# Performance work log

Measured on AMD Instinct MI355X. Metric: run time of the kernel, lower is better.

The kernel has to match this reference:

```python
import jax, jax.numpy as jnp
import numpy as np

D = 512; H = 8; DH = D // H; DFF = 4 * D; INNER = 2 * D; K = 31
B = 8; S = 1024
EPS = 1e-5


def layer_norm(x, g, b):
    m = jnp.mean(x, axis=-1, keepdims=True)
    v = jnp.mean(jnp.square(x - m), axis=-1, keepdims=True)
    return (x - m) * jax.lax.rsqrt(v + EPS) * g + b


def setup_inputs() -> dict:
    key = jax.random.key(0)
    ks = iter(jax.random.split(key, 32))
    w = lambda *s: jax.random.normal(next(ks), s, dtype=jnp.float32) * 0.02
    d = {
        "x": jax.random.normal(next(ks), (B, S, D), dtype=jnp.float32),
        # FF module 1
        "ln1_g": jnp.ones((D,)), "ln1_b": jnp.zeros((D,)),
        "ff1_w1": w(DFF, D), "ff1_b1": jnp.zeros((DFF,)),
        "ff1_w2": w(D, DFF), "ff1_b2": jnp.zeros((D,)),
        # attention
        "lna_g": jnp.ones((D,)), "lna_b": jnp.zeros((D,)),
        "qkv_w": w(3 * D, D), "qkv_b": jnp.zeros((3 * D,)),
        "out_w": w(D, D), "out_b": jnp.zeros((D,)),
        # conv module
        "lnc_g": jnp.ones((D,)), "lnc_b": jnp.zeros((D,)),
        "pw1_w": w(INNER, D), "pw1_b": jnp.zeros((INNER,)),
        "dw_w": w(D, 1, K), "dw_b": jnp.zeros((D,)),
        "bn_g": jnp.ones((D,)), "bn_b": jnp.zeros((D,)),
        "bn_mean": jnp.zeros((D,)), "bn_var": jnp.ones((D,)),
        "pw2_w": w(D, D), "pw2_b": jnp.zeros((D,)),
        # FF module 2
        "ln2_g": jnp.ones((D,)), "ln2_b": jnp.zeros((D,)),
        "ff2_w1": w(DFF, D), "ff2_b1": jnp.zeros((DFF,)),
        "ff2_w2": w(D, DFF), "ff2_b2": jnp.zeros((D,)),
        # final layer norm
        "lnf_g": jnp.ones((D,)), "lnf_b": jnp.zeros((D,)),
    }
    return d


def _ff(x, g, b, w1, b1, w2, b2):
    h = layer_norm(x, g, b)
    h = jax.nn.silu(h @ w1.T + b1)
    h = h @ w2.T + b2
    return h + x  # FeedForwardModule adds its own residual


def _attn(x, g, b, qkv_w, qkv_b, out_w, out_b):
    h = layer_norm(x, g, b)
    qkv = (h @ qkv_w.T + qkv_b).reshape(B, S, 3, H, DH)
    q, k, v = qkv[:, :, 0], qkv[:, :, 1], qkv[:, :, 2]  # [B,S,H,DH]
    scores = jnp.einsum('bqhd,bkhd->bhqk', q, k) / np.sqrt(DH).astype(np.float32)
    probs = jax.nn.softmax(scores, axis=-1)
    ctx = jnp.einsum('bhqk,bkhd->bqhd', probs, v).reshape(B, S, D)
    return ctx @ out_w.T + out_b


def _conv(x, g, b, pw1_w, pw1_b, dw_w, dw_b, bn_g, bn_b, bn_mean, bn_var, pw2_w, pw2_b):
    h = layer_norm(x, g, b)
    y = h @ pw1_w.T + pw1_b                      # [B,S,2D] pointwise conv1
    a, gate = jnp.split(y, 2, axis=-1)           # GLU along channel dim
    y = a * jax.nn.sigmoid(gate)                 # [B,S,D]
    y = y.transpose(0, 2, 1)                     # [B,D,S]
    y = jax.lax.conv_general_dilated(
        y, dw_w, window_strides=(1,), padding=((K // 2, K // 2),),
        dimension_numbers=('NCH', 'OIH', 'NCH'), feature_group_count=D)
    y = y + dw_b[None, :, None]
    y = (y - bn_mean[None, :, None]) * jax.lax.rsqrt(bn_var + EPS)[None, :, None]
    y = y * bn_g[None, :, None] + bn_b[None, :, None]
    y = jax.nn.silu(y)
    y = y.transpose(0, 2, 1)                     # [B,S,D]
    y = y @ pw2_w.T + pw2_b
    return y + x  # ConvModule adds its own residual


def reference(x, ln1_g, ln1_b, ff1_w1, ff1_b1, ff1_w2, ff1_b2,
              lna_g, lna_b, qkv_w, qkv_b, out_w, out_b,
              lnc_g, lnc_b, pw1_w, pw1_b, dw_w, dw_b,
              bn_g, bn_b, bn_mean, bn_var, pw2_w, pw2_b,
              ln2_g, ln2_b, ff2_w1, ff2_b1, ff2_w2, ff2_b2,
              lnf_g, lnf_b):
    x = x + 0.5 * _ff(x, ln1_g, ln1_b, ff1_w1, ff1_b1, ff1_w2, ff1_b2)
    x = x + _attn(x, lna_g, lna_b, qkv_w, qkv_b, out_w, out_b)
    x = x + _conv(x, lnc_g, lnc_b, pw1_w, pw1_b, dw_w, dw_b,
                  bn_g, bn_b, bn_mean, bn_var, pw2_w, pw2_b)
    x = x + 0.5 * _ff(x, ln2_g, ln2_b, ff2_w1, ff2_b1, ff2_w2, ff2_b2)
    return layer_norm(x, lnf_g, lnf_b)
```

## Files before the change

### kernel.cpp

```cpp
#include <hip/hip_runtime.h>
#include <hip/hip_bf16.h>

typedef __attribute__((ext_vector_type(8))) short bf16x8;
typedef __attribute__((ext_vector_type(4))) float f32x4;

#define NTOK 8192
#define SEQ  1024
#define NH   8

__device__ __forceinline__ float bfs2f(short s) {
  union { unsigned u; float f; } x; x.u = ((unsigned)(unsigned short)s) << 16; return x.f;
}
__device__ __forceinline__ short f2bfs(float f) {
  __hip_bfloat16 h = __float2bfloat16(f);
  return *reinterpret_cast<short*>(&h);
}
__device__ __forceinline__ float bfp2f(const __hip_bfloat16* p) {
  return bfs2f(*reinterpret_cast<const short*>(p));
}

__device__ __forceinline__ void gld16(const void* g, void* l) {
  __builtin_amdgcn_global_load_lds(
      (__attribute__((address_space(1))) void*)const_cast<void*>(g),
      (__attribute__((address_space(3))) void*)l, 16, 0, 0);
}

struct WSeg { const float* src; unsigned dst_off; unsigned nvec; };
struct WPack { WSeg s[8]; };

__global__ __launch_bounds__(256) void cast_wall_kernel(WPack p,
                                                        __hip_bfloat16* __restrict__ dst) {
  unsigned v = blockIdx.x * 256 + threadIdx.x;
#pragma unroll
  for (int t = 0; t < 8; ++t) {
    if (v < p.s[t].nvec) {
      const float* s = p.s[t].src + (size_t)v * 8;
      f32x4 a = *reinterpret_cast<const f32x4*>(s);
      f32x4 b = *reinterpret_cast<const f32x4*>(s + 4);
      bf16x8 o;
#pragma unroll
      for (int j = 0; j < 4; ++j) { o[j] = f2bfs(a[j]); o[4 + j] = f2bfs(b[j]); }
      *reinterpret_cast<bf16x8*>(reinterpret_cast<short*>(dst) +
                                 (size_t)(p.s[t].dst_off + v) * 8) = o;
      return;
    }
    v -= p.s[t].nvec;
  }
}

__global__ __launch_bounds__(256) void cast_dww_kernel(const float* __restrict__ src,
                                                       __hip_bfloat16* __restrict__ dst) {
  for (int k = 0; k < 31; ++k)
    for (int c = threadIdx.x; c < 512; c += 256)
      dst[k * 512 + c] = __float2bfloat16(src[c * 31 + k]);
}

struct PtrPack { const void* p[23]; };

__global__ __launch_bounds__(256) void cast_small_kernel(PtrPack pk,
                                                         __hip_bfloat16* __restrict__ dst) {
  constexpr int sizes[23] = {512, 512, 2048, 512, 512, 512, 1536, 512, 512, 512, 1024, 512,
                             512, 512, 512, 512, 512, 512, 512, 2048, 512, 512, 512};
  int off = 0;
  for (int t = 0; t < 23; ++t) {
    const int n = sizes[t];
    for (int i = threadIdx.x; i < n; i += 256)
      dst[off + i] = __float2bfloat16(((const float*)pk.p[t])[i]);
    off += n;
  }
}

__global__ void ws_bad_kernel(float* __restrict__ out) {
  if (threadIdx.x == 0) out[0] = 5000.f;
}

__global__ __launch_bounds__(256) void ln_kernel(const float* __restrict__ in,
                                                 const __hip_bfloat16* __restrict__ g,
                                                 const __hip_bfloat16* __restrict__ b,
                                                 __hip_bfloat16* __restrict__ out) {
  const int wv = threadIdx.x >> 6, ln = threadIdx.x & 63;
  const int row = blockIdx.x * 4 + wv;
  const float* p = in + (size_t)row * 512 + ln * 8;
  float v[8];
  {
    const f32x4* p4 = reinterpret_cast<const f32x4*>(p);
    f32x4 a = p4[0], c = p4[1];
#pragma unroll
    for (int j = 0; j < 4; ++j) { v[j] = a[j]; v[4 + j] = c[j]; }
  }
  float s = 0.f;
#pragma unroll
  for (int j = 0; j < 8; ++j) s += v[j];
  for (int m = 1; m < 64; m <<= 1) s += __shfl_xor(s, m);
  const float mean = s * (1.f / 512.f);
  float q = 0.f;
#pragma unroll
  for (int j = 0; j < 8; ++j) { float d = v[j] - mean; q += d * d; }
  for (int m = 1; m < 64; m <<= 1) q += __shfl_xor(q, m);
  const float rstd = rsqrtf(q * (1.f / 512.f) + 1e-5f);
  bf16x8 gg = *reinterpret_cast<const bf16x8*>(g + ln * 8);
  bf16x8 bb = *reinterpret_cast<const bf16x8*>(b + ln * 8);
  bf16x8 ov;
#pragma unroll
  for (int j = 0; j < 8; ++j)
    ov[j] = f2bfs((v[j] - mean) * rstd * bfs2f(gg[j]) + bfs2f(bb[j]));
  *reinterpret_cast<bf16x8*>(out + (size_t)row * 512 + ln * 8) = ov;
}

__global__ __launch_bounds__(256) void lnf_kernel(const float* __restrict__ in,
                                                  const __hip_bfloat16* __restrict__ g,
                                                  const __hip_bfloat16* __restrict__ b,
                                                  float* __restrict__ out) {
  const int wv = threadIdx.x >> 6, ln = threadIdx.x & 63;
  const int row = blockIdx.x * 4 + wv;
  const float* p = in + (size_t)row * 512 + ln * 8;
  float v[8];
  {
    const f32x4* p4 = reinterpret_cast<const f32x4*>(p);
    f32x4 a = p4[0], c = p4[1];
#pragma unroll
    for (int j = 0; j < 4; ++j) { v[j] = a[j]; v[4 + j] = c[j]; }
  }
  float s = 0.f;
#pragma unroll
  for (int j = 0; j < 8; ++j) s += v[j];
  for (int m = 1; m < 64; m <<= 1) s += __shfl_xor(s, m);
  const float mean = s * (1.f / 512.f);
  float q = 0.f;
#pragma unroll
  for (int j = 0; j < 8; ++j) { float d = v[j] - mean; q += d * d; }
  for (int m = 1; m < 64; m <<= 1) q += __shfl_xor(q, m);
  const float rstd = rsqrtf(q * (1.f / 512.f) + 1e-5f);
  bf16x8 gg = *reinterpret_cast<const bf16x8*>(g + ln * 8);
  bf16x8 bb = *reinterpret_cast<const bf16x8*>(b + ln * 8);
  f32x4 o0, o1;
#pragma unroll
  for (int j = 0; j < 4; ++j) {
    o0[j] = (v[j] - mean) * rstd * bfs2f(gg[j]) + bfs2f(bb[j]);
    o1[j] = (v[4 + j] - mean) * rstd * bfs2f(gg[4 + j]) + bfs2f(bb[4 + j]);
  }
  float* op = out + (size_t)row * 512 + ln * 8;
  *reinterpret_cast<f32x4*>(op) = o0;
  *reinterpret_cast<f32x4*>(op + 4) = o1;
}

template <int EPI>
__global__ __launch_bounds__(256, 2) void gemm_bt(const __hip_bfloat16* __restrict__ A,
                                                  const __hip_bfloat16* __restrict__ W,
                                                  const __hip_bfloat16* __restrict__ bias,
                                                  __hip_bfloat16* __restrict__ outb,
                                                  float* __restrict__ resid,
                                                  int K, int M, float alpha, float beta) {
  __shared__ __align__(16) __hip_bfloat16 As[128 * 64];
  __shared__ __align__(16) __hip_bfloat16 Bs[128 * 64];
  const int tid = threadIdx.x;
  const int wv = tid >> 6, ln = tid & 63;
  const int hi = ln >> 4, lo = ln & 15;
  const int lo7 = lo & 7;
  const int gx = gridDim.x;
  const int nwg = gx * gridDim.y;
  const int t = blockIdx.y * gx + blockIdx.x;
  const int w = (t & 7) * (nwg >> 3) + (t >> 3);
  const int n0 = (w & (gx - 1)) * 128;
  const int m0 = (w / gx) * 128;
  const int wr = wv >> 1, wc = wv & 1;
  const int srow = ln >> 3;
  const int scolz = (((ln & 7) ^ srow) << 3);

  f32x4 acc[4][4] = {};

  for (int k0 = 0; k0 < K; k0 += 64) {
    __syncthreads();
#pragma unroll
    for (int i = 0; i < 4; ++i) {
      const int grp = i * 4 + wv;
      const int row = grp * 8 + srow;
      gld16(A + (size_t)(n0 + row) * K + k0 + scolz, As + grp * 512);
      gld16(W + (size_t)(m0 + row) * K + k0 + scolz, Bs + grp * 512);
    }
    __syncthreads();
#pragma unroll
    for (int kk2 = 0; kk2 < 2; ++kk2) {
      const int g0 = ((kk2 * 4 + hi) ^ lo7) << 3;
      bf16x8 af[4], bfr[4];
#pragma unroll
      for (int r = 0; r < 4; ++r)
        af[r] = *reinterpret_cast<const bf16x8*>(As + (wr * 64 + r * 16 + lo) * 64 + g0);
#pragma unroll
      for (int c = 0; c < 4; ++c)
        bfr[c] = *reinterpret_cast<const bf16x8*>(Bs + (wc * 64 + c * 16 + lo) * 64 + g0);
#pragma unroll
      for (int r = 0; r < 4; ++r)
#pragma unroll
        for (int c = 0; c < 4; ++c)
          acc[r][c] = __builtin_amdgcn_mfma_f32_16x16x32_bf16(af[r], bfr[c], acc[r][c], 0, 0, 0);
    }
  }

#pragma unroll
  for (int r = 0; r < 4; ++r) {
#pragma unroll
    for (int c = 0; c < 4; ++c) {
      const int m = m0 + wc * 64 + c * 16 + lo;
      const float bv = bfp2f(bias + m);
#pragma unroll
      for (int j = 0; j < 4; ++j) {
        const int n = n0 + wr * 64 + r * 16 + hi * 4 + j;
        float v = acc[r][c][j] + bv;
        if constexpr (EPI == 1) v = v / (1.f + __expf(-v));
        if constexpr (EPI <= 1) {
          outb[(size_t)n * M + m] = __float2bfloat16(v);
        } else {
          const size_t idx = (size_t)n * 512 + m;
          resid[idx] = alpha * resid[idx] + beta * v;
        }
      }
    }
  }
}

__global__ __launch_bounds__(256, 4) void gemm64_resid(const __hip_bfloat16* __restrict__ A,
                                                       const __hip_bfloat16* __restrict__ W,
                                                       const __hip_bfloat16* __restrict__ bias,
                                                       const float* __restrict__ rsrc,
                                                       float* __restrict__ resid,
                                                       int K, float alpha, float beta) {
  __shared__ __align__(16) __hip_bfloat16 As[64 * 64];
  __shared__ __align__(16) __hip_bfloat16 Bs[128 * 64];
  const int tid = threadIdx.x;
  const int wv = tid >> 6, ln = tid & 63;
  const int hi = ln >> 4, lo = ln & 15;
  const int lo7 = lo & 7;
  const int gx = gridDim.x;
  const int nwg = gx * gridDim.y;
  const int t = blockIdx.y * gx + blockIdx.x;
  const int w = (t & 7) * (nwg >> 3) + (t >> 3);
  const int n0 = (w & (gx - 1)) * 64;
  const int m0 = (w / gx) * 128;
  const int wr = wv >> 1, wc = wv & 1;
  const int srow = ln >> 3;
  const int scolz = (((ln & 7) ^ srow) << 3);

  f32x4 acc[2][4] = {};

  for (int k0 = 0; k0 < K; k0 += 64) {
    __syncthreads();
#pragma unroll
    for (int i = 0; i < 2; ++i) {
      const int grp = i * 4 + wv;
      gld16(A + (size_t)(n0 + grp * 8 + srow) * K + k0 + scolz, As + grp * 512);
    }
#pragma unroll
    for (int i = 0; i < 4; ++i) {
      const int grp = i * 4 + wv;
      gld16(W + (size_t)(m0 + grp * 8 + srow) * K + k0 + scolz, Bs + grp * 512);
    }
    __syncthreads();
#pragma unroll
    for (int kk2 = 0; kk2 < 2; ++kk2) {
      const int g0 = ((kk2 * 4 + hi) ^ lo7) << 3;
      bf16x8 af[2], bfr[4];
#pragma unroll
      for (int r = 0; r < 2; ++r)
        af[r] = *reinterpret_cast<const bf16x8*>(As + (wr * 32 + r * 16 + lo) * 64 + g0);
#pragma unroll
      for (int c = 0; c < 4; ++c)
        bfr[c] = *reinterpret_cast<const bf16x8*>(Bs + (wc * 64 + c * 16 + lo) * 64 + g0);
#pragma unroll
      for (int r = 0; r < 2; ++r)
#pragma unroll
        for (int c = 0; c < 4; ++c)
          acc[r][c] = __builtin_amdgcn_mfma_f32_16x16x32_bf16(af[r], bfr[c], acc[r][c], 0, 0, 0);
    }
  }

#pragma unroll
  for (int r = 0; r < 2; ++r) {
#pragma unroll
    for (int c = 0; c < 4; ++c) {
      const int m = m0 + wc * 64 + c * 16 + lo;
      const float bv = bfp2f(bias + m);
#pragma unroll
      for (int j = 0; j < 4; ++j) {
        const int n = n0 + wr * 32 + r * 16 + hi * 4 + j;
        const size_t idx = (size_t)n * 512 + m;
        resid[idx] = alpha * rsrc[idx] + beta * (acc[r][c][j] + bv);
      }
    }
  }
}

__global__ __launch_bounds__(256, 1) void naive_attn_kernel(
    const __hip_bfloat16* __restrict__ qkv, __hip_bfloat16* __restrict__ ctx) {
  const int idx = blockIdx.x * 256 + threadIdx.x;
  const int b = idx >> 13;
  const int h = (idx >> 10) & 7;
  const int q = idx & 1023;
  const __hip_bfloat16* qp = qkv + (size_t)(b * SEQ + q) * 1536 + h * 64;
  float qreg[64];
#pragma unroll
  for (int j8 = 0; j8 < 8; ++j8) {
    bf16x8 v = *reinterpret_cast<const bf16x8*>(qp + j8 * 8);
#pragma unroll
    for (int jj = 0; jj < 8; ++jj) qreg[j8 * 8 + jj] = bfs2f(v[jj]);
  }
  float m = -1e30f, l = 0.f;
  float acc[64];
#pragma unroll
  for (int d = 0; d < 64; ++d) acc[d] = 0.f;
  for (int k = 0; k < SEQ; ++k) {
    const __hip_bfloat16* kp = qkv + (size_t)(b * SEQ + k) * 1536 + 512 + h * 64;
    float dot = 0.f;
#pragma unroll
    for (int j8 = 0; j8 < 8; ++j8) {
      bf16x8 v = *reinterpret_cast<const bf16x8*>(kp + j8 * 8);
#pragma unroll
      for (int jj = 0; jj < 8; ++jj) dot += qreg[j8 * 8 + jj] * bfs2f(v[jj]);
    }
    const float s = dot * 0.125f;
    const float nm = fmaxf(m, s);
    const float resc = __expf(m - nm);
    const float p = __expf(s - nm);
    l = l * resc + p;
    const __hip_bfloat16* vp = qkv + (size_t)(b * SEQ + k) * 1536 + 1024 + h * 64;
#pragma unroll
    for (int j8 = 0; j8 < 8; ++j8) {
      bf16x8 v = *reinterpret_cast<const bf16x8*>(vp + j8 * 8);
#pragma unroll
      for (int jj = 0; jj < 8; ++jj)
        acc[j8 * 8 + jj] = acc[j8 * 8 + jj] * resc + p * bfs2f(v[jj]);
    }
    m = nm;
  }
  __hip_bfloat16* op = ctx + (size_t)(b * SEQ + q) * 512 + h * 64;
  const float rl = 1.f / l;
#pragma unroll
  for (int j8 = 0; j8 < 8; ++j8) {
    bf16x8 o;
#pragma unroll
    for (int jj = 0; jj < 8; ++jj) o[jj] = f2bfs(acc[j8 * 8 + jj] * rl);
    *reinterpret_cast<bf16x8*>(op + j8 * 8) = o;
  }
}

__global__ __launch_bounds__(256) void vtrans_kernel(const __hip_bfloat16* __restrict__ qkv,
                                                     __hip_bfloat16* __restrict__ vT) {
  __shared__ __hip_bfloat16 tile[64][65];
  const int bh = blockIdx.x;
  const int s0 = blockIdx.y * 64;
  const int b = bh >> 3, h = bh & 7;
  const int c = threadIdx.x & 63;
  const int r4 = threadIdx.x >> 6;
#pragma unroll
  for (int i = 0; i < 16; ++i) {
    const int s = r4 * 16 + i;
    tile[s][c] = qkv[(size_t)(b * 1024 + s0 + s) * 1536 + 1024 + h * 64 + c];
  }
  __syncthreads();
#pragma unroll
  for (int i = 0; i < 16; ++i) {
    const int d = r4 * 16 + i;
    vT[((size_t)bh * 64 + d) * 1024 + s0 + c] = tile[c][d];
  }
}

__global__ __launch_bounds__(256, 4) void attn_kernel(const __hip_bfloat16* __restrict__ qkv,
                                                      const __hip_bfloat16* __restrict__ vT,
                                                      __hip_bfloat16* __restrict__ ctx) {
  __shared__ __align__(16) short Ks[2][64 * 64];
  __shared__ __align__(16) short Vs[2][64 * 64];
  __shared__ __align__(16) short P[4][16][64];
  const int tid = threadIdx.x;
  const int wv = tid >> 6, ln = tid & 63;
  const int hi = ln >> 4, lo = ln & 15;
  const int lo7 = lo & 7;
  const int blk = ((blockIdx.x & 7) << 7) | (blockIdx.x >> 3);
  const int qt = blk & 15, h = (blk >> 4) & 7, b = blk >> 7;
  const int q0 = qt * 64 + wv * 16;

  const int srow8 = ln >> 3;
  const int gsrc = (ln & 7) ^ srow8;

  bf16x8 aq0, aq1;
  {
    const __hip_bfloat16* qp = qkv + (size_t)(b * SEQ + q0 + lo) * 1536 + h * 64 + hi * 8;
    bf16x8 r0 = *reinterpret_cast<const bf16x8*>(qp);
    bf16x8 r1 = *reinterpret_cast<const bf16x8*>(qp + 32);
#pragma unroll
    for (int j = 0; j < 8; ++j) {
      aq0[j] = f2bfs(bfs2f(r0[j]) * 0.125f);
      aq1[j] = f2bfs(bfs2f(r1[j]) * 0.125f);
    }
  }

  const __hip_bfloat16* kbase = qkv + 512 + h * 64 + (size_t)b * SEQ * 1536;
  const __hip_bfloat16* vbase = vT + (size_t)(b * NH + h) * 64 * 1024;

  f32x4 oacc[4] = {};
  float lrow[4] = {0.f, 0.f, 0.f, 0.f};

#pragma unroll
  for (int c = 0; c < 2; ++c) {
    const int r = c * 32 + wv * 8 + srow8;
    gld16(kbase + (size_t)r * 1536 + gsrc * 8, &Ks[0][(c * 32 + wv * 8) * 64]);
    gld16(vbase + (size_t)r * 1024 + gsrc * 8, &Vs[0][(c * 32 + wv * 8) * 64]);
  }
  __syncthreads();

  int cb = 0;
  for (int kt = 0; kt < 16; ++kt) {
    if (kt < 15) {
      const int kb2 = (kt + 1) * 64;
#pragma unroll
      for (int c = 0; c < 2; ++c) {
        const int r = c * 32 + wv * 8 + srow8;
        gld16(kbase + (size_t)(kb2 + r) * 1536 + gsrc * 8,
              &Ks[cb ^ 1][(c * 32 + wv * 8) * 64]);
        gld16(vbase + (size_t)r * 1024 + kb2 + gsrc * 8,
              &Vs[cb ^ 1][(c * 32 + wv * 8) * 64]);
      }
    }

    f32x4 sc[4] = {};
#pragma unroll
    for (int nt = 0; nt < 4; ++nt) {
      const short* kr = &Ks[cb][(nt * 16 + lo) * 64];
      bf16x8 bk0 = *reinterpret_cast<const bf16x8*>(kr + ((hi ^ lo7) << 3));
      bf16x8 bk1 = *reinterpret_cast<const bf16x8*>(kr + (((hi + 4) ^ lo7) << 3));
      sc[nt] = __builtin_amdgcn_mfma_f32_16x16x32_bf16(aq0, bk0, sc[nt], 0, 0, 0);
      sc[nt] = __builtin_amdgcn_mfma_f32_16x16x32_bf16(aq1, bk1, sc[nt], 0, 0, 0);
    }

#pragma unroll
    for (int j = 0; j < 4; ++j) {
      const int prow = hi * 4 + j;
      const int pswz = (prow & 7) << 3;
#pragma unroll
      for (int nt = 0; nt < 4; ++nt) {
        const float p = __expf(sc[nt][j]);
        P[wv][prow][(nt * 16 + lo) ^ pswz] = f2bfs(p);
        lrow[j] += p;
      }
    }
    asm volatile("" ::: "memory");

    const short* pr = &P[wv][lo][0];
    bf16x8 ap0 = *reinterpret_cast<const bf16x8*>(pr + ((hi ^ lo7) << 3));
    bf16x8 ap1 = *reinterpret_cast<const bf16x8*>(pr + (((hi + 4) ^ lo7) << 3));
#pragma unroll
    for (int dt = 0; dt < 4; ++dt) {
      const short* vr = &Vs[cb][(dt * 16 + lo) * 64];
      bf16x8 bv0 = *reinterpret_cast<const bf16x8*>(vr + ((hi ^ lo7) << 3));
      bf16x8 bv1 = *reinterpret_cast<const bf16x8*>(vr + (((hi + 4) ^ lo7) << 3));
      oacc[dt] = __builtin_amdgcn_mfma_f32_16x16x32_bf16(ap0, bv0, oacc[dt], 0, 0, 0);
      oacc[dt] = __builtin_amdgcn_mfma_f32_16x16x32_bf16(ap1, bv1, oacc[dt], 0, 0, 0);
    }
    __syncthreads();
    cb ^= 1;
  }

#pragma unroll
  for (int j = 0; j < 4; ++j) {
    float s = lrow[j];
    s += __shfl_xor(s, 1);
    s += __shfl_xor(s, 2);
    s += __shfl_xor(s, 4);
    s += __shfl_xor(s, 8);
    lrow[j] = s;
  }

#pragma unroll
  for (int dt = 0; dt < 4; ++dt)
#pragma unroll
    for (int j = 0; j < 4; ++j) {
      const int n = b * SEQ + q0 + hi * 4 + j;
      const int d = h * 64 + dt * 16 + lo;
      ctx[(size_t)n * 512 + d] = __float2bfloat16(oacc[dt][j] / lrow[j]);
    }
}

__global__ __launch_bounds__(256) void glu8_kernel(const __hip_bfloat16* __restrict__ y,
                                                   __hip_bfloat16* __restrict__ o) {
  const int i = blockIdx.x * 256 + threadIdx.x;
  const int c8 = i & 63;
  const int n = i >> 6;
  const short* yp = reinterpret_cast<const short*>(y) + (size_t)n * 1024 + c8 * 8;
  bf16x8 a = *reinterpret_cast<const bf16x8*>(yp);
  bf16x8 g = *reinterpret_cast<const bf16x8*>(yp + 512);
  bf16x8 ov;
#pragma unroll
  for (int j = 0; j < 8; ++j) {
    const float av = bfs2f(a[j]);
    const float gv = bfs2f(g[j]);
    ov[j] = f2bfs(av / (1.f + __expf(-gv)));
  }
  *reinterpret_cast<bf16x8*>(reinterpret_cast<short*>(o) + (size_t)n * 512 + c8 * 8) = ov;
}

__global__ __launch_bounds__(256) void dwconv8_kernel(const __hip_bfloat16* __restrict__ cin,
                                                      const __hip_bfloat16* __restrict__ wkT,
                                                      const __hip_bfloat16* __restrict__ cb,
                                                      const __hip_bfloat16* __restrict__ bng,
                                                      const __hip_bfloat16* __restrict__ bnb,
                                                      const __hip_bfloat16* __restrict__ bnm,
                                                      const __hip_bfloat16* __restrict__ bnv,
                                                      __hip_bfloat16* __restrict__ outp) {
  const int i = blockIdx.x * 256 + threadIdx.x;
  const int c8 = i & 63;
  const int n = i >> 6;
  const int t = n & 1023;
  const int base = n - t;
  const int co = c8 * 8;

  float acc[8];
  {
    bf16x8 bv = *reinterpret_cast<const bf16x8*>(cb + co);
#pragma unroll
    for (int j = 0; j < 8; ++j) acc[j] = bfs2f(bv[j]);
  }
  const int k0 = (t >= 15) ? 0 : (15 - t);
  const int k1 = (t <= SEQ - 16) ? 31 : (SEQ - 1 - t + 16);
  const short* cin_s = reinterpret_cast<const short*>(cin);
  const short* wk_s = reinterpret_cast<const short*>(wkT);
  for (int k = k0; k < k1; ++k) {
    const int ts = t + k - 15;
    bf16x8 xv = *reinterpret_cast<const bf16x8*>(cin_s + (((size_t)(base + ts)) << 9) + co);
    bf16x8 wv = *reinterpret_cast<const bf16x8*>(wk_s + k * 512 + co);
#pragma unroll
    for (int j = 0; j < 8; ++j) acc[j] += bfs2f(xv[j]) * bfs2f(wv[j]);
  }
  bf16x8 g = *reinterpret_cast<const bf16x8*>(bng + co);
  bf16x8 bb = *reinterpret_cast<const bf16x8*>(bnb + co);
  bf16x8 bm = *reinterpret_cast<const bf16x8*>(bnm + co);
  bf16x8 bvv = *reinterpret_cast<const bf16x8*>(bnv + co);
  bf16x8 ov;
#pragma unroll
  for (int j = 0; j < 8; ++j) {
    const float scl = bfs2f(g[j]) * rsqrtf(bfs2f(bvv[j]) + 1e-5f);
    float v = (acc[j] - bfs2f(bm[j])) * scl + bfs2f(bb[j]);
    v = v / (1.f + __expf(-v));
    ov[j] = f2bfs(v);
  }
  *reinterpret_cast<bf16x8*>(reinterpret_cast<short*>(outp) + ((size_t)n << 9) + co) = ov;
}

extern "C" void kernel_launch(void* const* d_in, const int* in_sizes, int n_in,
                              void* d_out, int out_size, void* d_ws, size_t ws_size,
                              hipStream_t stream) {
  float* out = (float*)d_out;
  if (ws_size < ((size_t)80 << 20)) {
    ws_bad_kernel<<<1, 64, 0, stream>>>(out);
    return;
  }

  const float* x = (const float*)d_in[0];

  char* ws = (char*)d_ws;
  float*          xs = (float*)ws;
  __hip_bfloat16* t0 = (__hip_bfloat16*)(ws + ((size_t)16 << 20));
  __hip_bfloat16* t1 = (__hip_bfloat16*)(ws + ((size_t)24 << 20));
  __hip_bfloat16* t2 = (__hip_bfloat16*)(ws + ((size_t)56 << 20));
  __hip_bfloat16* wc = (__hip_bfloat16*)(ws + ((size_t)64 << 20));
  __hip_bfloat16* vT = t1 + (size_t)NTOK * 1536;

  __hip_bfloat16* wc_ff1_w1 = wc + 0;
  __hip_bfloat16* wc_ff1_w2 = wc + 1048576;
  __hip_bfloat16* wc_qkv_w  = wc + 2097152;
  __hip_bfloat16* wc_out_w  = wc + 2883584;
  __hip_bfloat16* wc_pw1_w  = wc + 3145728;
  __hip_bfloat16* wc_pw2_w  = wc + 3670016;
  __hip_bfloat16* wc_ff2_w1 = wc + 3932160;
  __hip_bfloat16* wc_ff2_w2 = wc + 4980736;
  __hip_bfloat16* wc_dwT    = wc + 6029312;
  __hip_bfloat16* sm        = wc + 6045184;
  __hip_bfloat16* c_ln1_g = sm + 0,     *c_ln1_b = sm + 512,   *c_ff1_b1 = sm + 1024;
  __hip_bfloat16* c_ff1_b2 = sm + 3072, *c_lna_g = sm + 3584,  *c_lna_b = sm + 4096;
  __hip_bfloat16* c_qkv_b = sm + 4608,  *c_out_b = sm + 6144,  *c_lnc_g = sm + 6656;
  __hip_bfloat16* c_lnc_b = sm + 7168,  *c_pw1_b = sm + 7680,  *c_dw_b = sm + 8704;
  __hip_bfloat16* c_bn_g = sm + 9216,   *c_bn_b = sm + 9728,   *c_bn_m = sm + 10240;
  __hip_bfloat16* c_bn_v = sm + 10752,  *c_pw2_b = sm + 11264, *c_ln2_g = sm + 11776;
  __hip_bfloat16* c_ln2_b = sm + 12288, *c_ff2_b1 = sm + 12800, *c_ff2_b2 = sm + 14848;
  __hip_bfloat16* c_lnf_g = sm + 15360, *c_lnf_b = sm + 15872;

  {
    WPack wp;
    wp.s[0] = {(const float*)d_in[3],  0,      131072};
    wp.s[1] = {(const float*)d_in[5],  131072, 131072};
    wp.s[2] = {(const float*)d_in[9],  262144, 98304};
    wp.s[3] = {(const float*)d_in[11], 360448, 32768};
    wp.s[4] = {(const float*)d_in[15], 393216, 65536};
    wp.s[5] = {(const float*)d_in[23], 458752, 32768};
    wp.s[6] = {(const float*)d_in[27], 491520, 131072};
    wp.s[7] = {(const float*)d_in[29], 622592, 131072};
    cast_wall_kernel<<<2944, 256, 0, stream>>>(wp, wc);
  }
  cast_dww_kernel<<<1, 256, 0, stream>>>((const float*)d_in[17], wc_dwT);
  PtrPack pk;
  const int small_idx[23] = {1, 2, 4, 6, 7, 8, 10, 12, 13, 14, 16, 18,
                             19, 20, 21, 22, 24, 25, 26, 28, 30, 31, 32};
  for (int t = 0; t < 23; ++t) pk.p[t] = d_in[small_idx[t]];
  cast_small_kernel<<<1, 256, 0, stream>>>(pk, sm);

  ln_kernel<<<2048, 256, 0, stream>>>(x, c_ln1_g, c_ln1_b, t0);
  gemm_bt<1><<<dim3(64, 16), 256, 0, stream>>>(t0, wc_ff1_w1, c_ff1_b1, t1, nullptr, 512, 2048, 0.f, 0.f);
  gemm64_resid<<<dim3(128, 4), 256, 0, stream>>>(t1, wc_ff1_w2, c_ff1_b2, x, xs, 2048, 1.5f, 0.5f);

  ln_kernel<<<2048, 256, 0, stream>>>(xs, c_lna_g, c_lna_b, t0);
  gemm_bt<0><<<dim3(64, 12), 256, 0, stream>>>(t0, wc_qkv_w, c_qkv_b, t1, nullptr, 512, 1536, 0.f, 0.f);
  vtrans_kernel<<<dim3(64, 16), 256, 0, stream>>>(t1, vT);
  attn_kernel<<<1024, 256, 0, stream>>>(t1, vT, t2);
  gemm64_resid<<<dim3(128, 4), 256, 0, stream>>>(t2, wc_out_w, c_out_b, xs, xs, 512, 1.0f, 1.0f);

  ln_kernel<<<2048, 256, 0, stream>>>(xs, c_lnc_g, c_lnc_b, t0);
  gemm_bt<0><<<dim3(64, 8), 256, 0, stream>>>(t0, wc_pw1_w, c_pw1_b, t1, nullptr, 512, 1024, 0.f, 0.f);
  glu8_kernel<<<2048, 256, 0, stream>>>(t1, t2);
  dwconv8_kernel<<<2048, 256, 0, stream>>>(t2, wc_dwT, c_dw_b, c_bn_g, c_bn_b, c_bn_m, c_bn_v, t0);
  gemm64_resid<<<dim3(128, 4), 256, 0, stream>>>(t0, wc_pw2_w, c_pw2_b, xs, xs, 512, 2.0f, 1.0f);

  ln_kernel<<<2048, 256, 0, stream>>>(xs, c_ln2_g, c_ln2_b, t0);
  gemm_bt<1><<<dim3(64, 16), 256, 0, stream>>>(t0, wc_ff2_w1, c_ff2_b1, t1, nullptr, 512, 2048, 0.f, 0.f);
  gemm64_resid<<<dim3(128, 4), 256, 0, stream>>>(t1, wc_ff2_w2, c_ff2_b2, xs, xs, 2048, 1.5f, 0.5f);

  lnf_kernel<<<2048, 256, 0, stream>>>(xs, c_lnf_g, c_lnf_b, out);
}
```

Measured before the change: 304.9 us.

## Process two query tiles per attention block to reuse K/V tiles

The attention kernel now has each wave handle two 16-row query tiles, 128 queries per block, so each K/V tile staged in LDS and held in registers is used twice. The grid is halved to 512 blocks and launch bounds are lowered to 2 blocks per SM to make room for the extra accumulators. This is meant to cut LDS and global traffic per unit of work, at the cost of more registers and fewer resident blocks. The GEMM launch bound is raised to 3, and the unused naive attention kernel is removed.

Measured after the change: 303.3 us. Within noise of the previous version (-0.5%).

```diff
diff --git a/kernel.cpp b/kernel.cpp
--- a/kernel.cpp
+++ b/kernel.cpp
@@ -145,7 +145,7 @@
 }
 
 template <int EPI>
-__global__ __launch_bounds__(256, 2) void gemm_bt(const __hip_bfloat16* __restrict__ A,
+__global__ __launch_bounds__(256, 3) void gemm_bt(const __hip_bfloat16* __restrict__ A,
                                                   const __hip_bfloat16* __restrict__ W,
                                                   const __hip_bfloat16* __restrict__ bias,
                                                   __hip_bfloat16* __restrict__ outb,
@@ -290,59 +290,6 @@
   }
 }
 
-__global__ __launch_bounds__(256, 1) void naive_attn_kernel(
-    const __hip_bfloat16* __restrict__ qkv, __hip_bfloat16* __restrict__ ctx) {
-  const int idx = blockIdx.x * 256 + threadIdx.x;
-  const int b = idx >> 13;
-  const int h = (idx >> 10) & 7;
-  const int q = idx & 1023;
-  const __hip_bfloat16* qp = qkv + (size_t)(b * SEQ + q) * 1536 + h * 64;
-  float qreg[64];
-#pragma unroll
-  for (int j8 = 0; j8 < 8; ++j8) {
-    bf16x8 v = *reinterpret_cast<const bf16x8*>(qp + j8 * 8);
-#pragma unroll
-    for (int jj = 0; jj < 8; ++jj) qreg[j8 * 8 + jj] = bfs2f(v[jj]);
-  }
-  float m = -1e30f, l = 0.f;
-  float acc[64];
-#pragma unroll
-  for (int d = 0; d < 64; ++d) acc[d] = 0.f;
-  for (int k = 0; k < SEQ; ++k) {
-    const __hip_bfloat16* kp = qkv + (size_t)(b * SEQ + k) * 1536 + 512 + h * 64;
-    float dot = 0.f;
-#pragma unroll
-    for (int j8 = 0; j8 < 8; ++j8) {
-      bf16x8 v = *reinterpret_cast<const bf16x8*>(kp + j8 * 8);
-#pragma unroll
-      for (int jj = 0; jj < 8; ++jj) dot += qreg[j8 * 8 + jj] * bfs2f(v[jj]);
-    }
-    const float s = dot * 0.125f;
-    const float nm = fmaxf(m, s);
-    const float resc = __expf(m - nm);
-    const float p = __expf(s - nm);
-    l = l * resc + p;
-    const __hip_bfloat16* vp = qkv + (size_t)(b * SEQ + k) * 1536 + 1024 + h * 64;
-#pragma unroll
-    for (int j8 = 0; j8 < 8; ++j8) {
-      bf16x8 v = *reinterpret_cast<const bf16x8*>(vp + j8 * 8);
-#pragma unroll
-      for (int jj = 0; jj < 8; ++jj)
-        acc[j8 * 8 + jj] = acc[j8 * 8 + jj] * resc + p * bfs2f(v[jj]);
-    }
-    m = nm;
-  }
-  __hip_bfloat16* op = ctx + (size_t)(b * SEQ + q) * 512 + h * 64;
-  const float rl = 1.f / l;
-#pragma unroll
-  for (int j8 = 0; j8 < 8; ++j8) {
-    bf16x8 o;
-#pragma unroll
-    for (int jj = 0; jj < 8; ++jj) o[jj] = f2bfs(acc[j8 * 8 + jj] * rl);
-    *reinterpret_cast<bf16x8*>(op + j8 * 8) = o;
-  }
-}
-
 __global__ __launch_bounds__(256) void vtrans_kernel(const __hip_bfloat16* __restrict__ qkv,
                                                      __hip_bfloat16* __restrict__ vT) {
   __shared__ __hip_bfloat16 tile[64][65];
@@ -364,7 +311,7 @@
   }
 }
 
-__global__ __launch_bounds__(256, 4) void attn_kernel(const __hip_bfloat16* __restrict__ qkv,
+__global__ __launch_bounds__(256, 2) void attn_kernel(const __hip_bfloat16* __restrict__ qkv,
                                                       const __hip_bfloat16* __restrict__ vT,
                                                       __hip_bfloat16* __restrict__ ctx) {
   __shared__ __align__(16) short Ks[2][64 * 64];
@@ -374,30 +321,36 @@
   const int wv = tid >> 6, ln = tid & 63;
   const int hi = ln >> 4, lo = ln & 15;
   const int lo7 = lo & 7;
-  const int blk = ((blockIdx.x & 7) << 7) | (blockIdx.x >> 3);
-  const int qt = blk & 15, h = (blk >> 4) & 7, b = blk >> 7;
-  const int q0 = qt * 64 + wv * 16;
+  const int blk = ((blockIdx.x & 7) << 6) | (blockIdx.x >> 3);
+  const int qt = blk & 7, h = (blk >> 3) & 7, b = blk >> 6;
+  const int q0 = qt * 128 + wv * 16;
 
   const int srow8 = ln >> 3;
   const int gsrc = (ln & 7) ^ srow8;
 
-  bf16x8 aq0, aq1;
+  bf16x8 aq0a, aq1a, aq0b, aq1b;
   {
-    const __hip_bfloat16* qp = qkv + (size_t)(b * SEQ + q0 + lo) * 1536 + h * 64 + hi * 8;
-    bf16x8 r0 = *reinterpret_cast<const bf16x8*>(qp);
-    bf16x8 r1 = *reinterpret_cast<const bf16x8*>(qp + 32);
+    const __hip_bfloat16* qpa = qkv + (size_t)(b * SEQ + q0 + lo) * 1536 + h * 64 + hi * 8;
+    const __hip_bfloat16* qpb = qpa + (size_t)64 * 1536;
+    bf16x8 r0 = *reinterpret_cast<const bf16x8*>(qpa);
+    bf16x8 r1 = *reinterpret_cast<const bf16x8*>(qpa + 32);
+    bf16x8 r2 = *reinterpret_cast<const bf16x8*>(qpb);
+    bf16x8 r3 = *reinterpret_cast<const bf16x8*>(qpb + 32);
 #pragma unroll
     for (int j = 0; j < 8; ++j) {
-      aq0[j] = f2bfs(bfs2f(r0[j]) * 0.125f);
-      aq1[j] = f2bfs(bfs2f(r1[j]) * 0.125f);
+      aq0a[j] = f2bfs(bfs2f(r0[j]) * 0.125f);
+      aq1a[j] = f2bfs(bfs2f(r1[j]) * 0.125f);
+      aq0b[j] = f2bfs(bfs2f(r2[j]) * 0.125f);
+      aq1b[j] = f2bfs(bfs2f(r3[j]) * 0.125f);
     }
   }
 
   const __hip_bfloat16* kbase = qkv + 512 + h * 64 + (size_t)b * SEQ * 1536;
   const __hip_bfloat16* vbase = vT + (size_t)(b * NH + h) * 64 * 1024;
 
-  f32x4 oacc[4] = {};
-  float lrow[4] = {0.f, 0.f, 0.f, 0.f};
+  f32x4 oaccA[4] = {}, oaccB[4] = {};
+  float lrowA[4] = {0.f, 0.f, 0.f, 0.f};
+  float lrowB[4] = {0.f, 0.f, 0.f, 0.f};
 
 #pragma unroll
   for (int c = 0; c < 2; ++c) {
@@ -421,14 +374,28 @@
       }
     }
 
-    f32x4 sc[4] = {};
+    bf16x8 bk0[4], bk1[4];
 #pragma unroll
     for (int nt = 0; nt < 4; ++nt) {
       const short* kr = &Ks[cb][(nt * 16 + lo) * 64];
-      bf16x8 bk0 = *reinterpret_cast<const bf16x8*>(kr + ((hi ^ lo7) << 3));
-      bf16x8 bk1 = *reinterpret_cast<const bf16x8*>(kr + (((hi + 4) ^ lo7) << 3));
-      sc[nt] = __builtin_amdgcn_mfma_f32_16x16x32_bf16(aq0, bk0, sc[nt], 0, 0, 0);
-      sc[nt] = __builtin_amdgcn_mfma_f32_16x16x32_bf16(aq1, bk1, sc[nt], 0, 0, 0);
+      bk0[nt] = *reinterpret_cast<const bf16x8*>(kr + ((hi ^ lo7) << 3));
+      bk1[nt] = *reinterpret_cast<const bf16x8*>(kr + (((hi + 4) ^ lo7) << 3));
+    }
+    f32x4 scA[4] = {}, scB[4] = {};
+#pragma unroll
+    for (int nt = 0; nt < 4; ++nt) {
+      scA[nt] = __builtin_amdgcn_mfma_f32_16x16x32_bf16(aq0a, bk0[nt], scA[nt], 0, 0, 0);
+      scA[nt] = __builtin_amdgcn_mfma_f32_16x16x32_bf16(aq1a, bk1[nt], scA[nt], 0, 0, 0);
+      scB[nt] = __builtin_amdgcn_mfma_f32_16x16x32_bf16(aq0b, bk0[nt], scB[nt], 0, 0, 0);
+      scB[nt] = __builtin_amdgcn_mfma_f32_16x16x32_bf16(aq1b, bk1[nt], scB[nt], 0, 0, 0);
+    }
+
+    bf16x8 bv0[4], bv1[4];
+#pragma unroll
+    for (int dt = 0; dt < 4; ++dt) {
+      const short* vr = &Vs[cb][(dt * 16 + lo) * 64];
+      bv0[dt] = *reinterpret_cast<const bf16x8*>(vr + ((hi ^ lo7) << 3));
+      bv1[dt] = *reinterpret_cast<const bf16x8*>(vr + (((hi + 4) ^ lo7) << 3));
     }
 
 #pragma unroll
@@ -437,23 +404,45 @@
       const int pswz = (prow & 7) << 3;
 #pragma unroll
       for (int nt = 0; nt < 4; ++nt) {
-        const float p = __expf(sc[nt][j]);
+        const float p = __expf(scA[nt][j]);
         P[wv][prow][(nt * 16 + lo) ^ pswz] = f2bfs(p);
-        lrow[j] += p;
+        lrowA[j] += p;
       }
     }
     asm volatile("" ::: "memory");
-
-    const short* pr = &P[wv][lo][0];
-    bf16x8 ap0 = *reinterpret_cast<const bf16x8*>(pr + ((hi ^ lo7) << 3));
-    bf16x8 ap1 = *reinterpret_cast<const bf16x8*>(pr + (((hi + 4) ^ lo7) << 3));
-#pragma unroll
-    for (int dt = 0; dt < 4; ++dt) {
-      const short* vr = &Vs[cb][(dt * 16 + lo) * 64];
-      bf16x8 bv0 = *reinterpret_cast<const bf16x8*>(vr + ((hi ^ lo7) << 3));
-      bf16x8 bv1 = *reinterpret_cast<const bf16x8*>(vr + (((hi + 4) ^ lo7) << 3));
-      oacc[dt] = __builtin_amdgcn_mfma_f32_16x16x32_bf16(ap0, bv0, oacc[dt], 0, 0, 0);
-      oacc[dt] = __builtin_amdgcn_mfma_f32_16x16x32_bf16(ap1, bv1, oacc[dt], 0, 0, 0);
+    {
+      const short* pr = &P[wv][lo][0];
+      bf16x8 ap0 = *reinterpret_cast<const bf16x8*>(pr + ((hi ^ lo7) << 3));
+      bf16x8 ap1 = *reinterpret_cast<const bf16x8*>(pr + (((hi + 4) ^ lo7) << 3));
+#pragma unroll
+      for (int dt = 0; dt < 4; ++dt) {
+        oaccA[dt] = __builtin_amdgcn_mfma_f32_16x16x32_bf16(ap0, bv0[dt], oaccA[dt], 0, 0, 0);
+        oaccA[dt] = __builtin_amdgcn_mfma_f32_16x16x32_bf16(ap1, bv1[dt], oaccA[dt], 0, 0, 0);
+      }
+    }
+    asm volatile("" ::: "memory");
+
+#pragma unroll
+    for (int j = 0; j < 4; ++j) {
+      const int prow = hi * 4 + j;
+      const int pswz = (prow & 7) << 3;
+#pragma unroll
+      for (int nt = 0; nt < 4; ++nt) {
+        const float p = __expf(scB[nt][j]);
+        P[wv][prow][(nt * 16 + lo) ^ pswz] = f2bfs(p);
+        lrowB[j] += p;
+      }
+    }
+    asm volatile("" ::: "memory");
+    {
+      const short* pr = &P[wv][lo][0];
+      bf16x8 ap0 = *reinterpret_cast<const bf16x8*>(pr + ((hi ^ lo7) << 3));
+      bf16x8 ap1 = *reinterpret_cast<const bf16x8*>(pr + (((hi + 4) ^ lo7) << 3));
+#pragma unroll
+      for (int dt = 0; dt < 4; ++dt) {
+        oaccB[dt] = __builtin_amdgcn_mfma_f32_16x16x32_bf16(ap0, bv0[dt], oaccB[dt], 0, 0, 0);
+        oaccB[dt] = __builtin_amdgcn_mfma_f32_16x16x32_bf16(ap1, bv1[dt], oaccB[dt], 0, 0, 0);
+      }
     }
     __syncthreads();
     cb ^= 1;
@@ -461,21 +450,23 @@
 
 #pragma unroll
   for (int j = 0; j < 4; ++j) {
-    float s = lrow[j];
-    s += __shfl_xor(s, 1);
-    s += __shfl_xor(s, 2);
-    s += __shfl_xor(s, 4);
-    s += __shfl_xor(s, 8);
-    lrow[j] = s;
+    float sa = lrowA[j], sb = lrowB[j];
+    sa += __shfl_xor(sa, 1); sb += __shfl_xor(sb, 1);
+    sa += __shfl_xor(sa, 2); sb += __shfl_xor(sb, 2);
+    sa += __shfl_xor(sa, 4); sb += __shfl_xor(sb, 4);
+    sa += __shfl_xor(sa, 8); sb += __shfl_xor(sb, 8);
+    lrowA[j] = sa; lrowB[j] = sb;
   }
 
 #pragma unroll
   for (int dt = 0; dt < 4; ++dt)
 #pragma unroll
     for (int j = 0; j < 4; ++j) {
-      const int n = b * SEQ + q0 + hi * 4 + j;
       const int d = h * 64 + dt * 16 + lo;
-      ctx[(size_t)n * 512 + d] = __float2bfloat16(oacc[dt][j] / lrow[j]);
+      const int na = b * SEQ + q0 + hi * 4 + j;
+      ctx[(size_t)na * 512 + d] = __float2bfloat16(oaccA[dt][j] / lrowA[j]);
+      const int nb = na + 64;
+      ctx[(size_t)nb * 512 + d] = __float2bfloat16(oaccB[dt][j] / lrowB[j]);
     }
 }
 
@@ -608,7 +599,7 @@
   ln_kernel<<<2048, 256, 0, stream>>>(xs, c_lna_g, c_lna_b, t0);
   gemm_bt<0><<<dim3(64, 12), 256, 0, stream>>>(t0, wc_qkv_w, c_qkv_b, t1, nullptr, 512, 1536, 0.f, 0.f);
   vtrans_kernel<<<dim3(64, 16), 256, 0, stream>>>(t1, vT);
-  attn_kernel<<<1024, 256, 0, stream>>>(t1, vT, t2);
+  attn_kernel<<<512, 256, 0, stream>>>(t1, vT, t2);
   gemm64_resid<<<dim3(128, 4), 256, 0, stream>>>(t2, wc_out_w, c_out_b, xs, xs, 512, 1.0f, 1.0f);
 
   ln_kernel<<<2048, 256, 0, stream>>>(xs, c_lnc_g, c_lnc_b, t0);
```
